# Kernel optimization log

Hardware: AMD Instinct MI355X
Metric: run time of the kernel (lower is better)

Reference implementation:

```python
import jax, jax.numpy as jnp
import numpy as np

NBODY = 63          # body 0 = world, body 1 = free-joint root, bodies 2..62 = hinge
NHINGE = NBODY - 2  # 61 hinge dofs -> qpos dim = 7 + 61 = 68
NSITES = 16
B = 131072


def _qmul(q1, q2):
    """Hamilton product, (w,x,y,z) convention. Broadcasts over leading dims."""
    w1, x1, y1, z1 = q1[..., 0], q1[..., 1], q1[..., 2], q1[..., 3]
    w2, x2, y2, z2 = q2[..., 0], q2[..., 1], q2[..., 2], q2[..., 3]
    return jnp.stack([
        w1 * w2 - x1 * x2 - y1 * y2 - z1 * z2,
        w1 * x2 + x1 * w2 + y1 * z2 - z1 * y2,
        w1 * y2 - x1 * z2 + y1 * w2 + z1 * x2,
        w1 * z2 + x1 * y2 - y1 * x2 + z1 * w2,
    ], axis=-1)


def _qrot(q, v):
    """Rotate v by unit quaternion q (equivalent to q*v*q^-1 sandwich)."""
    u = q[..., 1:]
    w = q[..., :1]
    t = 2.0 * jnp.cross(u, v)
    return v + w * t + jnp.cross(u, t)


def setup_inputs() -> dict:
    key = jax.random.key(0)
    ks = jax.random.split(key, 8)
    qpos = jax.random.normal(ks[0], (B, 7 + NHINGE), dtype=jnp.float32) * 0.3
    body_pos = jax.random.normal(ks[1], (NBODY, 3), dtype=jnp.float32) * 0.1
    bq = jax.random.normal(ks[2], (NBODY, 4), dtype=jnp.float32)
    body_quat = bq / jnp.linalg.norm(bq, axis=-1, keepdims=True)
    ax = jax.random.normal(ks[3], (NHINGE, 3), dtype=jnp.float32)
    hinge_axis = ax / jnp.linalg.norm(ax, axis=-1, keepdims=True)
    jnt_pos = jax.random.normal(ks[4], (NHINGE, 3), dtype=jnp.float32) * 0.05
    site_pos = jax.random.normal(ks[5], (NSITES, 3), dtype=jnp.float32) * 0.05
    body_parent = jnp.maximum(jnp.arange(NBODY, dtype=jnp.int32) - 1, 0)  # chain tree
    site_body = jax.random.randint(ks[6], (NSITES,), 1, NBODY, dtype=jnp.int32)
    return {
        'qpos': qpos, 'body_pos': body_pos, 'body_quat': body_quat,
        'hinge_axis': hinge_axis, 'jnt_pos': jnt_pos, 'site_pos': site_pos,
        'body_parent': body_parent, 'site_body': site_body,
    }


def reference(qpos, body_pos, body_quat, hinge_axis, jnt_pos, site_pos,
              body_parent, site_body):
    # Structural ints are static tree topology: pull to host for Python indexing.
    parents = np.asarray(body_parent)
    sbody = np.asarray(site_body)
    Bn = qpos.shape[0]
    nbody = body_pos.shape[0]

    wp = [None] * nbody  # per-body world position [B,3]
    wq = [None] * nbody  # per-body world quaternion [B,4]
    wp[0] = jnp.zeros((Bn, 3), dtype=qpos.dtype)
    wq[0] = jnp.broadcast_to(jnp.array([1.0, 0.0, 0.0, 0.0], dtype=qpos.dtype), (Bn, 4))

    # body 1: free joint -> root pos + normalized quat straight from qpos
    wp[1] = qpos[:, 0:3]
    q = qpos[:, 3:7]
    wq[1] = q / jnp.linalg.norm(q, axis=-1, keepdims=True)

    # hinge bodies, parents always processed before children
    for bid in range(2, nbody):
        h = bid - 2
        p = int(parents[bid])
        half = 0.5 * qpos[:, 7 + h]
        s, c = jnp.sin(half), jnp.cos(half)
        ax = hinge_axis[h]
        hq = jnp.stack([c, s * ax[0], s * ax[1], s * ax[2]], axis=-1)  # [B,4]
        local_combined = _qmul(jnp.broadcast_to(body_quat[bid], (Bn, 4)), hq)
        anchor = wp[p] + _qrot(wq[p], body_pos[bid] + jnt_pos[h])  # world joint anchor
        nq = _qmul(wq[p], local_combined)
        wq[bid] = nq
        wp[bid] = anchor - _qrot(nq, jnt_pos[h])

    WP = jnp.stack(wp, axis=1)  # [B, nbody, 3]
    WQ = jnp.stack(wq, axis=1)  # [B, nbody, 4]

    # sites: vectorized gather + rotate over all keypoint sites at once
    sq = WQ[:, sbody]                         # [B, S, 4]
    sp = WP[:, sbody]                         # [B, S, 3]
    sites = sp + _qrot(sq, site_pos[None, :, :])  # [B, S, 3]
    return sites
```

## Files before the change

### kernel.cpp

```cpp
#include <hip/hip_runtime.h>


#define NBODY  63
#define NHINGE 61
#define NSITES 16
#define QDIM   68
#define LSTRIDE 49

typedef unsigned int u32;

#define HC_OFF   0
#define SP_OFF   (NHINGE * 16)
#define MASK_OFF (SP_OFF + NSITES * 4)
#define BM_OFF   (MASK_OFF + 64)

__global__ void fk_setup(const float* __restrict__ body_pos, const float* __restrict__ body_quat,
                         const float* __restrict__ hinge_axis, const float* __restrict__ jnt_pos,
                         const float* __restrict__ site_pos, const int* __restrict__ site_body,
                         float* __restrict__ ws)
{
    int tid = threadIdx.x;
    if (tid < NHINGE) {
        int h = tid, bid = h + 2;
        float uw = body_quat[bid*4+0], ux = body_quat[bid*4+1];
        float uy = body_quat[bid*4+2], uz = body_quat[bid*4+3];
        float ax = hinge_axis[h*3+0], ay = hinge_axis[h*3+1], az = hinge_axis[h*3+2];
        float jx = jnt_pos[h*3+0],   jy = jnt_pos[h*3+1],   jz = jnt_pos[h*3+2];
        float bx = body_pos[bid*3+0], by = body_pos[bid*3+1], bz = body_pos[bid*3+2];
        float* o = ws + HC_OFF + h * 16;
        o[0] = uw; o[1] = ux; o[2] = uy; o[3] = uz;
        o[4] = -(ux * ax + uy * ay + uz * az);
        o[5] =  uw * ax + uy * az - uz * ay;
        o[6] =  uw * ay - ux * az + uz * ax;
        o[7] =  uw * az + ux * ay - uy * ax;
        o[8] = bx + jx; o[9] = by + jy; o[10] = bz + jz; o[11] = 0.f;
        o[12] = jx; o[13] = jy; o[14] = jz; o[15] = 0.f;
    }
    if (tid < NSITES) {
        float* o = ws + SP_OFF + tid * 4;
        o[0] = site_pos[tid*3+0];
        o[1] = site_pos[tid*3+1];
        o[2] = site_pos[tid*3+2];
        o[3] = 0.f;
    }
    if (tid == 0) {
        int* im = (int*)(ws + MASK_OFF);
        unsigned long long bm = 0ull;
        for (int b = 0; b < NBODY; b++) {
            int m = 0;
            for (int s = 0; s < NSITES; s++)
                if (site_body[s] == b) m |= (1 << s);
            im[b] = m;
            if (m) bm |= (1ull << b);
        }
        u32* pbm = (u32*)(ws + BM_OFF);
        pbm[0] = (u32)bm; pbm[1] = (u32)(bm >> 32);
    }
}

__global__ __launch_bounds__(256, 2)
void fk_main(const float* __restrict__ qpos, const float* __restrict__ ws,
             float* __restrict__ out, int nb)
{
    __shared__ float sbuf[256 * LSTRIDE];
    const int tid = threadIdx.x;
    const int t = blockIdx.x * 256 + tid;
    float* my = sbuf + tid * LSTRIDE;

    if (t < nb) {
        float f[QDIM];
        const float4* q4 = reinterpret_cast<const float4*>(qpos) + (size_t)t * 17;
#pragma unroll
        for (int i = 0; i < 17; i++) {
            float4 v = q4[i];
            f[4*i+0] = v.x; f[4*i+1] = v.y; f[4*i+2] = v.z; f[4*i+3] = v.w;
        }

        const u32* pbm = (const u32*)(ws + BM_OFF);
        unsigned long long bodymask = ((unsigned long long)pbm[1] << 32) | (unsigned long long)pbm[0];
        const int* im = (const int*)(ws + MASK_OFF);

        float wpx = f[0], wpy = f[1], wpz = f[2];
        float qw = f[3], qx = f[4], qy = f[5], qz = f[6];
        float inv = rsqrtf(qw * qw + qx * qx + qy * qy + qz * qz);
        qw *= inv; qx *= inv; qy *= inv; qz *= inv;

        auto emit = [&](int bid) {
            int m = im[bid];
            while (m) {
                int s = __ffs(m) - 1; m &= m - 1;
                const float* sp = ws + SP_OFF + s * 4;
                float vx = sp[0], vy = sp[1], vz = sp[2];
                float tx = 2.f * (qy * vz - qz * vy);
                float ty = 2.f * (qz * vx - qx * vz);
                float tz = 2.f * (qx * vy - qy * vx);
                float* o = my + s * 3;
                o[0] = wpx + vx + qw * tx + (qy * tz - qz * ty);
                o[1] = wpy + vy + qw * ty + (qz * tx - qx * tz);
                o[2] = wpz + vz + qw * tz + (qx * ty - qy * tx);
            }
        };

        if (bodymask & 2ull) emit(1);

#pragma unroll
        for (int h = 0; h < NHINGE; h++) {
            const int bid = h + 2;
            const float* c = ws + HC_OFF + h * 16;
            float ang = 0.5f * f[7 + h];
            float sn, cs;
            __sincosf(ang, &sn, &cs);
            float lw = cs * c[0] + sn * c[4];
            float lx = cs * c[1] + sn * c[5];
            float ly = cs * c[2] + sn * c[6];
            float lz = cs * c[3] + sn * c[7];
            float ax = c[8], ay = c[9], az = c[10];
            float tx = 2.f * (qy * az - qz * ay);
            float ty = 2.f * (qz * ax - qx * az);
            float tz = 2.f * (qx * ay - qy * ax);
            float anx = wpx + ax + qw * tx + (qy * tz - qz * ty);
            float any_ = wpy + ay + qw * ty + (qz * tx - qx * tz);
            float anz = wpz + az + qw * tz + (qx * ty - qy * tx);
            float nw = qw * lw - qx * lx - qy * ly - qz * lz;
            float nx = qw * lx + qx * lw + qy * lz - qz * ly;
            float ny = qw * ly - qx * lz + qy * lw + qz * lx;
            float nz = qw * lz + qx * ly - qy * lx + qz * lw;
            float jx = c[12], jy = c[13], jz = c[14];
            float t2x = 2.f * (ny * jz - nz * jy);
            float t2y = 2.f * (nz * jx - nx * jz);
            float t2z = 2.f * (nx * jy - ny * jx);
            wpx = anx - (jx + nw * t2x + (ny * t2z - nz * t2y));
            wpy = any_ - (jy + nw * t2y + (nz * t2x - nx * t2z));
            wpz = anz - (jz + nw * t2z + (nx * t2y - ny * t2x));
            qw = nw; qx = nx; qy = ny; qz = nz;

            if (bodymask & (1ull << bid)) emit(bid);
        }
    }

    __syncthreads();

    {
        size_t blk_dw = (size_t)blockIdx.x * (256 * 48);
        if (blk_dw + 256 * 48 <= (size_t)nb * 48) {
            float4* out4 = reinterpret_cast<float4*>(out + blk_dw);
#pragma unroll
            for (int k = 0; k < 12; k++) {
                int g = k * 256 + tid;
                int q = g / 12;
                int r = (g - q * 12) * 4;
                const float* p = sbuf + q * LSTRIDE + r;
                float4 v = { p[0], p[1], p[2], p[3] };
                out4[g] = v;
            }
        }
    }
}

extern "C" void kernel_launch(void* const* d_in, const int* in_sizes, int n_in,
                              void* d_out, int out_size, void* d_ws, size_t ws_size,
                              hipStream_t stream)
{
    const float* qpos       = (const float*)d_in[0];
    const float* body_pos   = (const float*)d_in[1];
    const float* body_quat  = (const float*)d_in[2];
    const float* hinge_axis = (const float*)d_in[3];
    const float* jnt_pos    = (const float*)d_in[4];
    const float* site_pos   = (const float*)d_in[5];
    const int* site_body    = (const int*)d_in[7];
    float* ws = (float*)d_ws;

    int nb = in_sizes[0] / QDIM;

    fk_setup<<<1, 64, 0, stream>>>(body_pos, body_quat, hinge_axis, jnt_pos,
                                   site_pos, site_body, ws);
    fk_main<<<(nb + 255) / 256, 256, 0, stream>>>(qpos, ws, (float*)d_out, nb);
}
```

Baseline: 131.4 us.

## Fuse setup kernel into main kernel and stage constants in shared memory

Removes the separate single-block setup launch and has every block compute the per-hinge constants, site positions and site masks directly into shared memory after issuing its qpos loads. Constant reads in the hinge loop and emit now come from LDS instead of the global workspace, and one kernel launch plus its dependency are removed. The cost is redundant setup work in every block, one extra __syncthreads, and more LDS per block, which could affect occupancy. A scalar tail path for partial blocks is also added.

New measurement: 121.1 us. -7.9%, faster.

```diff
diff --git a/kernel.cpp b/kernel.cpp
--- a/kernel.cpp
+++ b/kernel.cpp
@@ -7,19 +7,36 @@
 #define QDIM   68
 #define LSTRIDE 49
 
-typedef unsigned int u32;
+__global__ __launch_bounds__(256, 2)
+void fk_main(const float* __restrict__ qpos,
+             const float* __restrict__ body_pos,
+             const float* __restrict__ body_quat,
+             const float* __restrict__ hinge_axis,
+             const float* __restrict__ jnt_pos,
+             const float* __restrict__ site_pos,
+             const int* __restrict__ site_body,
+             float* __restrict__ out, int nb)
+{
+    __shared__ float sbuf[256 * LSTRIDE];
+    __shared__ float hc[NHINGE][16];
+    __shared__ float spos[NSITES][4];
+    __shared__ int   smask[NBODY];
 
-#define HC_OFF   0
-#define SP_OFF   (NHINGE * 16)
-#define MASK_OFF (SP_OFF + NSITES * 4)
-#define BM_OFF   (MASK_OFF + 64)
+    const int tid = threadIdx.x;
+    const int t = blockIdx.x * 256 + tid;
+    float* my = sbuf + tid * LSTRIDE;
 
-__global__ void fk_setup(const float* __restrict__ body_pos, const float* __restrict__ body_quat,
-                         const float* __restrict__ hinge_axis, const float* __restrict__ jnt_pos,
-                         const float* __restrict__ site_pos, const int* __restrict__ site_body,
-                         float* __restrict__ ws)
-{
-    int tid = threadIdx.x;
+    float f[QDIM];
+    if (t < nb) {
+        const float4* q4 = reinterpret_cast<const float4*>(qpos) + (size_t)t * 17;
+#pragma unroll
+        for (int i = 0; i < 17; i++) {
+            float4 v = q4[i];
+            f[4*i+0] = v.x; f[4*i+1] = v.y; f[4*i+2] = v.z; f[4*i+3] = v.w;
+        }
+    }
+    __builtin_amdgcn_sched_barrier(0);
+
     if (tid < NHINGE) {
         int h = tid, bid = h + 2;
         float uw = body_quat[bid*4+0], ux = body_quat[bid*4+1];
@@ -27,70 +44,45 @@
         float ax = hinge_axis[h*3+0], ay = hinge_axis[h*3+1], az = hinge_axis[h*3+2];
         float jx = jnt_pos[h*3+0],   jy = jnt_pos[h*3+1],   jz = jnt_pos[h*3+2];
         float bx = body_pos[bid*3+0], by = body_pos[bid*3+1], bz = body_pos[bid*3+2];
-        float* o = ws + HC_OFF + h * 16;
-        o[0] = uw; o[1] = ux; o[2] = uy; o[3] = uz;
-        o[4] = -(ux * ax + uy * ay + uz * az);
-        o[5] =  uw * ax + uy * az - uz * ay;
-        o[6] =  uw * ay - ux * az + uz * ax;
-        o[7] =  uw * az + ux * ay - uy * ax;
-        o[8] = bx + jx; o[9] = by + jy; o[10] = bz + jz; o[11] = 0.f;
-        o[12] = jx; o[13] = jy; o[14] = jz; o[15] = 0.f;
+        hc[h][0] = uw; hc[h][1] = ux; hc[h][2] = uy; hc[h][3] = uz;
+        hc[h][4] = -(ux * ax + uy * ay + uz * az);
+        hc[h][5] =  uw * ax + uy * az - uz * ay;
+        hc[h][6] =  uw * ay - ux * az + uz * ax;
+        hc[h][7] =  uw * az + ux * ay - uy * ax;
+        hc[h][8] = bx + jx; hc[h][9] = by + jy; hc[h][10] = bz + jz; hc[h][11] = 0.f;
+        hc[h][12] = jx; hc[h][13] = jy; hc[h][14] = jz; hc[h][15] = 0.f;
     }
     if (tid < NSITES) {
-        float* o = ws + SP_OFF + tid * 4;
-        o[0] = site_pos[tid*3+0];
-        o[1] = site_pos[tid*3+1];
-        o[2] = site_pos[tid*3+2];
-        o[3] = 0.f;
+        spos[tid][0] = site_pos[tid*3+0];
+        spos[tid][1] = site_pos[tid*3+1];
+        spos[tid][2] = site_pos[tid*3+2];
+        spos[tid][3] = 0.f;
     }
-    if (tid == 0) {
-        int* im = (int*)(ws + MASK_OFF);
-        unsigned long long bm = 0ull;
-        for (int b = 0; b < NBODY; b++) {
-            int m = 0;
-            for (int s = 0; s < NSITES; s++)
-                if (site_body[s] == b) m |= (1 << s);
-            im[b] = m;
-            if (m) bm |= (1ull << b);
-        }
-        u32* pbm = (u32*)(ws + BM_OFF);
-        pbm[0] = (u32)bm; pbm[1] = (u32)(bm >> 32);
+    if (tid < NBODY) {
+        int m = 0;
+#pragma unroll
+        for (int s = 0; s < NSITES; s++)
+            m |= (site_body[s] == tid) ? (1 << s) : 0;
+        smask[tid] = m;
     }
-}
+    unsigned long long bodymask = 0ull;
+#pragma unroll
+    for (int s = 0; s < NSITES; s++)
+        bodymask |= 1ull << site_body[s];
 
-__global__ __launch_bounds__(256, 2)
-void fk_main(const float* __restrict__ qpos, const float* __restrict__ ws,
-             float* __restrict__ out, int nb)
-{
-    __shared__ float sbuf[256 * LSTRIDE];
-    const int tid = threadIdx.x;
-    const int t = blockIdx.x * 256 + tid;
-    float* my = sbuf + tid * LSTRIDE;
+    __syncthreads();
 
     if (t < nb) {
-        float f[QDIM];
-        const float4* q4 = reinterpret_cast<const float4*>(qpos) + (size_t)t * 17;
-#pragma unroll
-        for (int i = 0; i < 17; i++) {
-            float4 v = q4[i];
-            f[4*i+0] = v.x; f[4*i+1] = v.y; f[4*i+2] = v.z; f[4*i+3] = v.w;
-        }
-
-        const u32* pbm = (const u32*)(ws + BM_OFF);
-        unsigned long long bodymask = ((unsigned long long)pbm[1] << 32) | (unsigned long long)pbm[0];
-        const int* im = (const int*)(ws + MASK_OFF);
-
         float wpx = f[0], wpy = f[1], wpz = f[2];
         float qw = f[3], qx = f[4], qy = f[5], qz = f[6];
         float inv = rsqrtf(qw * qw + qx * qx + qy * qy + qz * qz);
         qw *= inv; qx *= inv; qy *= inv; qz *= inv;
 
         auto emit = [&](int bid) {
-            int m = im[bid];
+            int m = smask[bid];
             while (m) {
                 int s = __ffs(m) - 1; m &= m - 1;
-                const float* sp = ws + SP_OFF + s * 4;
-                float vx = sp[0], vy = sp[1], vz = sp[2];
+                float vx = spos[s][0], vy = spos[s][1], vz = spos[s][2];
                 float tx = 2.f * (qy * vz - qz * vy);
                 float ty = 2.f * (qz * vx - qx * vz);
                 float tz = 2.f * (qx * vy - qy * vx);
@@ -106,7 +98,7 @@
 #pragma unroll
         for (int h = 0; h < NHINGE; h++) {
             const int bid = h + 2;
-            const float* c = ws + HC_OFF + h * 16;
+            const float* c = hc[h];
             float ang = 0.5f * f[7 + h];
             float sn, cs;
             __sincosf(ang, &sn, &cs);
@@ -153,6 +145,8 @@
                 float4 v = { p[0], p[1], p[2], p[3] };
                 out4[g] = v;
             }
+        } else if (t < nb) {
+            for (int k = 0; k < 48; k++) out[(size_t)t * 48 + k] = my[k];
         }
     }
 }
@@ -168,11 +162,10 @@
     const float* jnt_pos    = (const float*)d_in[4];
     const float* site_pos   = (const float*)d_in[5];
     const int* site_body    = (const int*)d_in[7];
-    float* ws = (float*)d_ws;
 
     int nb = in_sizes[0] / QDIM;
 
-    fk_setup<<<1, 64, 0, stream>>>(body_pos, body_quat, hinge_axis, jnt_pos,
-                                   site_pos, site_body, ws);
-    fk_main<<<(nb + 255) / 256, 256, 0, stream>>>(qpos, ws, (float*)d_out, nb);
+    fk_main<<<(nb + 255) / 256, 256, 0, stream>>>(qpos, body_pos, body_quat,
+                                                  hinge_axis, jnt_pos, site_pos,
+                                                  site_body, (float*)d_out, nb);
 }
```
